# Kernel optimization log

Hardware: AMD Instinct MI355X
Metric: run time of the kernel (lower is better)

The kernel has to match this reference:

```python
import jax, jax.numpy as jnp
import numpy as np

N_EMBD = 1024
N_HEAD = 16


def setup_inputs() -> dict:
    key = jax.random.key(0)
    k1, k2, k3 = jax.random.split(key, 3)
    x = jax.random.normal(k1, (4, 2048, N_EMBD), dtype=jnp.float32)
    w_attn = jax.random.normal(k2, (N_EMBD, 3 * N_EMBD), dtype=jnp.float32) * (N_EMBD ** -0.5)
    w_proj = jax.random.normal(k3, (N_EMBD, N_EMBD), dtype=jnp.float32) * (N_EMBD ** -0.5)
    return {"x": x, "w_attn": w_attn, "w_proj": w_proj}


def reference(x, w_attn, w_proj):
    B, T, C = x.shape
    H = N_HEAD
    D = C // H  # head dim
    qkv = x @ w_attn  # [B,T,3C]
    q, k, v = jnp.split(qkv, 3, axis=-1)
    # [B,T,C] -> [B,H,T,D]
    q = q.reshape(B, T, H, D).transpose(0, 2, 1, 3)
    k = k.reshape(B, T, H, D).transpose(0, 2, 1, 3)
    v = v.reshape(B, T, H, D).transpose(0, 2, 1, 3)
    scale = 1.0 / jnp.sqrt(jnp.asarray(D, dtype=x.dtype))
    att = jnp.einsum('bhqd,bhkd->bhqk', q, k) * scale  # [B,H,T,T]
    causal = jnp.tril(jnp.ones((T, T), dtype=bool))
    att = jnp.where(causal, att, jnp.asarray(-jnp.inf, dtype=att.dtype))
    att = jax.nn.softmax(att, axis=-1)
    y = jnp.einsum('bhqk,bhkd->bhqd', att, v)  # [B,H,T,D]
    y = y.transpose(0, 2, 1, 3).reshape(B, T, C)
    return y @ w_proj
```

## Files before the change

### kernel.cpp

```cpp
#include <hip/hip_runtime.h>
#include <math.h>


typedef unsigned short ushort_t;
typedef __attribute__((ext_vector_type(8))) short bf16x8;
typedef __attribute__((ext_vector_type(4))) float f32x4;

#define MFMA16(a, b, c) __builtin_amdgcn_mfma_f32_16x16x32_bf16((a), (b), (c), 0, 0, 0)

#define CP_ASYNC16(lds, gp)                                                        \
    __builtin_amdgcn_global_load_lds(                                              \
        (const __attribute__((address_space(1))) void*)(gp),                       \
        (__attribute__((address_space(3))) void*)(lds), 16, 0, 0)

#define SCALE2 0.1803368801111204f

#define BAR() __builtin_amdgcn_s_barrier()
#define WAITBAR4()                                           \
    do {                                                     \
        asm volatile("s_waitcnt vmcnt(4)" ::: "memory");     \
        __builtin_amdgcn_s_barrier();                        \
    } while (0)
#define WAITBAR0()                                           \
    do {                                                     \
        asm volatile("s_waitcnt vmcnt(0)" ::: "memory");     \
        __builtin_amdgcn_s_barrier();                        \
    } while (0)

__device__ __forceinline__ ushort_t bf16r(float x) {
    unsigned int u = __float_as_uint(x);
    u += 0x7FFFu + ((u >> 16) & 1u);
    return (ushort_t)(u >> 16);
}

__device__ __forceinline__ unsigned cvt_pk_bf16(float lo, float hi) {
    unsigned r;
    asm("v_cvt_pk_bf16_f32 %0, %1, %2" : "=v"(r) : "v"(lo), "v"(hi));
    return r;
}
__device__ __forceinline__ void pl32_swap(unsigned& a, unsigned& c) {
    asm("v_permlane32_swap_b32 %0, %1" : "+v"(a), "+v"(c));
}
__device__ __forceinline__ void pl16_swap(unsigned& a, unsigned& c) {
    asm("v_permlane16_swap_b32 %0, %1" : "+v"(a), "+v"(c));
}


__global__ __launch_bounds__(256) void cast_f32_bf16(const float4* __restrict__ src,
                                                     ushort4* __restrict__ dst) {
    int i = blockIdx.x * 256 + threadIdx.x;
    float4 v = src[i];
    ushort4 o;
    o.x = bf16r(v.x); o.y = bf16r(v.y); o.z = bf16r(v.z); o.w = bf16r(v.w);
    dst[i] = o;
}

__global__ __launch_bounds__(256) void transpose_cast(const float* __restrict__ src,
                                                      ushort_t* __restrict__ dst,
                                                      int R, int Cc) {
    __shared__ float tile[32][33];
    const int tx = threadIdx.x, ty = threadIdx.y;
    const int c0 = blockIdx.x * 32, r0 = blockIdx.y * 32;
#pragma unroll
    for (int i = 0; i < 4; ++i)
        tile[ty + i * 8][tx] = src[(size_t)(r0 + ty + i * 8) * Cc + c0 + tx];
    __syncthreads();
#pragma unroll
    for (int i = 0; i < 4; ++i)
        dst[(size_t)(c0 + ty + i * 8) * R + r0 + tx] = bf16r(tile[tx][ty + i * 8]);
}

__global__ __launch_bounds__(512, 2)
void gemm256(const ushort_t* __restrict__ A, const ushort_t* __restrict__ Bt,
             int K, int mode,
             ushort_t* __restrict__ Qh, ushort_t* __restrict__ Kh,
             ushort_t* __restrict__ Vt, float* __restrict__ Cout, int nbx) {
    __shared__ __align__(16) ushort_t As[2][16384];
    __shared__ __align__(16) ushort_t Bs[2][16384];
    const int tid = threadIdx.x;
    const int l = tid & 63, w = tid >> 6;
    const int lm = l & 15, lq = l >> 4;
    const int wm = w >> 2, wn = w & 3;

    int bid = blockIdx.x;
    const int cpx = gridDim.x >> 3;
    bid = (bid & 7) * cpx + (bid >> 3);
    const int by = bid / nbx, bx = bid - by * nbx;
    const int row0 = by * 256, col0 = bx * 256;

    const int srow = tid >> 3, sslot = tid & 7;
    const int ssw = (sslot ^ (srow & 7)) * 8;
    const ushort_t* gA = A + (size_t)(row0 + srow) * K + ssw;
    const ushort_t* gB = Bt + (size_t)(col0 + srow) * K + ssw;

    auto stageA = [&](int dbuf, int hm, int T) {
        const ushort_t* s = gA + (size_t)(hm * 128) * K + T * 64;
        CP_ASYNC16(&As[dbuf][hm * 8192 + tid * 8], s);
        CP_ASYNC16(&As[dbuf][hm * 8192 + 4096 + tid * 8], s + (size_t)64 * K);
    };
    auto stageB = [&](int dbuf, int hm, int T) {
        const ushort_t* s = gB + (size_t)(hm * 128) * K + T * 64;
        CP_ASYNC16(&Bs[dbuf][hm * 8192 + tid * 8], s);
        CP_ASYNC16(&Bs[dbuf][hm * 8192 + 4096 + tid * 8], s + (size_t)64 * K);
    };

    const int arow0 = wm * 128 + lm;
    const int brow0 = wn * 64 + lm;
    const int lsw = lm & 7;

    f32x4 acc[8][4];
#pragma unroll
    for (int i = 0; i < 8; ++i)
#pragma unroll
        for (int j = 0; j < 4; ++j) acc[i][j] = (f32x4){0.f, 0.f, 0.f, 0.f};

    bf16x8 af[4][2];
    bf16x8 bq[2][2][2];

    auto ldA = [&](int d, int qm) {
#pragma unroll
        for (int mf = 0; mf < 4; ++mf) {
            const int r = arow0 + qm * 64 + mf * 16;
#pragma unroll
            for (int ks = 0; ks < 2; ++ks)
                af[mf][ks] =
                    *(const bf16x8*)(&As[d][r * 64 + (((ks << 2) | lq) ^ lsw) * 8]);
        }
    };
    auto ldB = [&](int d, int qn) {
#pragma unroll
        for (int nf = 0; nf < 2; ++nf) {
            const int r = brow0 + qn * 32 + nf * 16;
#pragma unroll
            for (int ks = 0; ks < 2; ++ks)
                bq[qn][nf][ks] =
                    *(const bf16x8*)(&Bs[d][r * 64 + (((ks << 2) | lq) ^ lsw) * 8]);
        }
    };
    auto mma = [&](int qm, int qn) {
        __builtin_amdgcn_s_setprio(1);
#pragma unroll
        for (int mf = 0; mf < 4; ++mf)
#pragma unroll
            for (int nf = 0; nf < 2; ++nf) {
                f32x4 c = acc[qm * 4 + mf][qn * 2 + nf];
                c = MFMA16(af[mf][0], bq[qn][nf][0], c);
                c = MFMA16(af[mf][1], bq[qn][nf][1], c);
                acc[qm * 4 + mf][qn * 2 + nf] = c;
            }
        __builtin_amdgcn_s_setprio(0);
    };

    stageA(0, 0, 0); stageA(0, 1, 0);
    stageB(0, 0, 0); stageB(0, 1, 0);
    stageB(1, 0, 1); stageB(1, 1, 1);

    const int ntiles = K >> 6;
    const int niter = ntiles >> 1;

    for (int it = 0; it < niter; ++it) {
        const int tE = 2 * it, tO = tE + 1;
        const bool s2 = (tE + 2) < ntiles;
        const bool s3 = (tE + 3) < ntiles;

        WAITBAR4();
        ldA(0, 0); ldB(0, 0);
        stageA(1, 0, tO);
        BAR();
        mma(0, 0);
        BAR();
        ldB(0, 1);
        stageA(1, 1, tO);
        BAR();
        mma(0, 1);
        BAR();
        ldA(0, 1);
        if (s2) stageB(0, 0, tE + 2);
        BAR();
        mma(1, 0);
        BAR();
        if (s2) stageB(0, 1, tE + 2);
        BAR();
        mma(1, 1);
        BAR();

        if (it + 1 < niter) { WAITBAR4(); } else { WAITBAR0(); }
        ldA(1, 0); ldB(1, 0);
        if (s2) stageA(0, 0, tE + 2);
        BAR();
        mma(0, 0);
        BAR();
        ldB(1, 1);
        if (s2) stageA(0, 1, tE + 2);
        BAR();
        mma(0, 1);
        BAR();
        ldA(1, 1);
        if (s3) stageB(1, 0, tE + 3);
        BAR();
        mma(1, 0);
        BAR();
        if (s3) stageB(1, 1, tE + 3);
        BAR();
        mma(1, 1);
        BAR();
    }

    if (mode == 1) {
#pragma unroll
        for (int im = 0; im < 8; ++im)
#pragma unroll
            for (int in = 0; in < 4; ++in)
#pragma unroll
                for (int reg = 0; reg < 4; ++reg) {
                    const int rr = row0 + wm * 128 + im * 16 + lq * 4 + reg;
                    const int cc = col0 + wn * 64 + in * 16 + lm;
                    Cout[(size_t)rr * 1024 + cc] = acc[im][in][reg];
                }
    } else {
#pragma unroll
        for (int im = 0; im < 8; ++im) {
#pragma unroll
            for (int in = 0; in < 4; ++in) {
#pragma unroll
                for (int reg = 0; reg < 4; ++reg) {
                    const int rr = row0 + wm * 128 + im * 16 + lq * 4 + reg;
                    const int cc = col0 + wn * 64 + in * 16 + lm;
                    const float v = acc[im][in][reg];
                    const int b = rr >> 11, t = rr & 2047;
                    if (cc < 1024) {
                        const int h = cc >> 6, d = cc & 63;
                        Qh[((size_t)(b * 16 + h) * 2048 + t) * 64 + d] =
                            bf16r(v * SCALE2);
                    } else if (cc < 2048) {
                        const int c2 = cc - 1024, h = c2 >> 6, d = c2 & 63;
                        Kh[((size_t)(b * 16 + h) * 2048 + t) * 64 + d] = bf16r(v);
                    } else {
                        const int c2 = cc - 2048, h = c2 >> 6, d = c2 & 63;
                        Vt[((size_t)(b * 16 + h) * 64 + d) * 2048 + t] = bf16r(v);
                    }
                }
            }
        }
    }
}

__global__ __launch_bounds__(256, 4)
void attn_mfma(const ushort_t* __restrict__ Qh, const ushort_t* __restrict__ Kh,
               const ushort_t* __restrict__ Vt, ushort_t* __restrict__ Y) {
    __shared__ ushort_t Ks[2][4096];
    __shared__ ushort_t Vs[2][4096];
    const int tid = threadIdx.x, l = tid & 63, w = tid >> 6;
    const int lm = l & 15, lq = l >> 4;
    const int bh = blockIdx.x;
    const int pr = blockIdx.y;
    const int qbA = pr, qbB = 31 - pr;
    const int b = bh >> 4, h = bh & 15;
    const f32x4 zero4 = {0.f, 0.f, 0.f, 0.f};
    const short oneb = (short)0x3F80;
    const bf16x8 onesf = {oneb, oneb, oneb, oneb, oneb, oneb, oneb, oneb};
    const int lqs8 = (lq ^ ((lm >> 1) & 3)) * 8;

    bf16x8 qf[2][2];
    {
        const ushort_t* qA = Qh + ((size_t)bh * 2048 + qbA * 64 + w * 16 + lm) * 64 + lq * 8;
        const ushort_t* qB = Qh + ((size_t)bh * 2048 + qbB * 64 + w * 16 + lm) * 64 + lq * 8;
        qf[0][0] = *(const bf16x8*)(qA);
        qf[0][1] = *(const bf16x8*)(qA + 32);
        qf[1][0] = *(const bf16x8*)(qB);
        qf[1][1] = *(const bf16x8*)(qB + 32);
    }

    f32x4 O[2][4], Ol[2];
#pragma unroll
    for (int q = 0; q < 2; ++q) {
        Ol[q] = zero4;
#pragma unroll
        for (int i = 0; i < 4; ++i) O[q][i] = zero4;
    }

    const int srow = tid >> 2, slot = tid & 3;
    const int srcoff = ((slot ^ ((srow >> 1) & 3)) * 8);
    const ushort_t* gKr = Kh + ((size_t)bh * 2048 + srow) * 64 + srcoff;
    const ushort_t* gVr = Vt + ((size_t)bh * 64 + srow) * 2048 + srcoff;

    auto prefetch = [&](int jbn, int dbuf) {
        const ushort_t* gk = gKr + (size_t)jbn * 4096;
        const ushort_t* gv = gVr + jbn * 64;
        CP_ASYNC16(&Ks[dbuf][tid * 8], gk);
        CP_ASYNC16(&Ks[dbuf][2048 + tid * 8], gk + 32);
        CP_ASYNC16(&Vs[dbuf][tid * 8], gv);
        CP_ASYNC16(&Vs[dbuf][2048 + tid * 8], gv + 32);
    };

    auto process = [&](const bf16x8 (&kf)[4][2], const ushort_t* Vb,
                       const bf16x8 (&qfr)[2], f32x4 (&Or)[4], f32x4& Olr,
                       bool diag) {
        f32x4 st[4];
        __builtin_amdgcn_s_setprio(1);
#pragma unroll
        for (int n = 0; n < 4; ++n) {
            f32x4 s_acc = zero4;
            s_acc = MFMA16(kf[n][0], qfr[0], s_acc);
            s_acc = MFMA16(kf[n][1], qfr[1], s_acc);
            st[n] = s_acc;
        }
        __builtin_amdgcn_s_setprio(0);

        float p[4][4];
#pragma unroll
        for (int n = 0; n < 4; ++n)
#pragma unroll
            for (int reg = 0; reg < 4; ++reg)
                p[n][reg] = __builtin_amdgcn_exp2f(st[n][reg]);
        if (diag) {
            const int qloc = w * 16 + lm;
#pragma unroll
            for (int n = 0; n < 4; ++n)
#pragma unroll
                for (int reg = 0; reg < 4; ++reg)
                    if (n * 16 + lq * 4 + reg > qloc) p[n][reg] = 0.f;
        }

        unsigned cpk[4][2];
#pragma unroll
        for (int n = 0; n < 4; ++n) {
            cpk[n][0] = cvt_pk_bf16(p[n][0], p[n][1]);
            cpk[n][1] = cvt_pk_bf16(p[n][2], p[n][3]);
        }

        union U8 { unsigned u[4]; bf16x8 v; };
        bf16x8 pf0, pf1;
        {
            unsigned z00 = cpk[0][0], z10 = cpk[1][0];
            unsigned z01 = cpk[0][1], z11 = cpk[1][1];
            pl32_swap(z00, z10); pl16_swap(z00, z10);
            pl32_swap(z01, z11); pl16_swap(z01, z11);
            U8 t0; t0.u[0] = z00; t0.u[1] = z01; t0.u[2] = z10; t0.u[3] = z11;
            pf0 = t0.v;
            unsigned y00 = cpk[2][0], y10 = cpk[3][0];
            unsigned y01 = cpk[2][1], y11 = cpk[3][1];
            pl32_swap(y00, y10); pl16_swap(y00, y10);
            pl32_swap(y01, y11); pl16_swap(y01, y11);
            U8 t1; t1.u[0] = y00; t1.u[1] = y01; t1.u[2] = y10; t1.u[3] = y11;
            pf1 = t1.v;
        }

        __builtin_amdgcn_s_setprio(1);
#pragma unroll
        for (int dn = 0; dn < 4; ++dn) {
            const bf16x8 vf0 = *(const bf16x8*)(Vb + (dn * 16 + lm) * 32 + lqs8);
            const bf16x8 vf1 = *(const bf16x8*)(Vb + 2048 + (dn * 16 + lm) * 32 + lqs8);
            Or[dn] = MFMA16(pf0, vf0, Or[dn]);
            Or[dn] = MFMA16(pf1, vf1, Or[dn]);
        }
        Olr = MFMA16(pf0, onesf, Olr);
        Olr = MFMA16(pf1, onesf, Olr);
        __builtin_amdgcn_s_setprio(0);
    };

    prefetch(0, 0);
    for (int jb = 0; jb <= qbB; ++jb) {
        const int buf = jb & 1;
        __syncthreads();
        if (jb < qbB) prefetch(jb + 1, buf ^ 1);

        const ushort_t* Kb = Ks[buf];
        const ushort_t* Vb = Vs[buf];
        bf16x8 kf[4][2];
#pragma unroll
        for (int n = 0; n < 4; ++n) {
            kf[n][0] = *(const bf16x8*)(Kb + (n * 16 + lm) * 32 + lqs8);
            kf[n][1] = *(const bf16x8*)(Kb + 2048 + (n * 16 + lm) * 32 + lqs8);
        }

        process(kf, Vb, qf[1], O[1], Ol[1], jb == qbB);
        if (jb <= qbA)
            process(kf, Vb, qf[0], O[0], Ol[0], jb == qbA);
    }

#pragma unroll
    for (int qs = 0; qs < 2; ++qs) {
        const int tq = (qs ? qbB : qbA) * 64;
#pragma unroll
        for (int reg = 0; reg < 4; ++reg) {
            const float inv = 1.f / Ol[qs][reg];
            const size_t row = (size_t)b * 2048 + tq + w * 16 + lq * 4 + reg;
#pragma unroll
            for (int dn = 0; dn < 4; ++dn)
                Y[row * 1024 + h * 64 + dn * 16 + lm] = bf16r(O[qs][dn][reg] * inv);
        }
    }
}


extern "C" void kernel_launch(void* const* d_in, const int* in_sizes, int n_in,
                              void* d_out, int out_size, void* d_ws, size_t ws_size,
                              hipStream_t stream) {
    const float* x      = (const float*)d_in[0];
    const float* w_attn = (const float*)d_in[1];
    const float* w_proj = (const float*)d_in[2];
    float* out = (float*)d_out;

    char* ws = (char*)d_ws;
    ushort_t* xb   = (ushort_t*)(ws);
    ushort_t* watT = (ushort_t*)(ws + 16777216);
    ushort_t* wpjT = (ushort_t*)(ws + 23068672);
    ushort_t* Qh   = (ushort_t*)(ws + 25165824);
    ushort_t* Kh   = (ushort_t*)(ws + 41943040);
    ushort_t* Vt   = (ushort_t*)(ws + 58720256);
    ushort_t* Y    = (ushort_t*)(ws + 75497472);

    hipLaunchKernelGGL(cast_f32_bf16, dim3(8192), dim3(256), 0, stream,
                       (const float4*)x, (ushort4*)xb);
    hipLaunchKernelGGL(transpose_cast, dim3(96, 32), dim3(32, 8), 0, stream,
                       w_attn, watT, 1024, 3072);
    hipLaunchKernelGGL(transpose_cast, dim3(32, 32), dim3(32, 8), 0, stream,
                       w_proj, wpjT, 1024, 1024);

    hipLaunchKernelGGL(gemm256, dim3(384), dim3(512), 0, stream,
                       xb, watT, 1024, 0, Qh, Kh, Vt, (float*)nullptr, 12);

    hipLaunchKernelGGL(attn_mfma, dim3(64, 16), dim3(256), 0, stream,
                       Qh, Kh, Vt, Y);

    hipLaunchKernelGGL(gemm256, dim3(128), dim3(512), 0, stream,
                       Y, wpjT, 1024, 1, (ushort_t*)nullptr, (ushort_t*)nullptr,
                       (ushort_t*)nullptr, out, 4);
}
```

Baseline: 263.3 us.

## Shrink GEMM tile to 256x128 with eight-phase pipeline to fill more CUs

Halves the GEMM block tile width from 256 to 128 columns, doubling the number of blocks for both the QKV and output projections, and restructures the wave layout and per-iteration phases (fewer barriers per K-tile). The aim is to occupy more compute units, especially for the output projection which previously launched only 128 blocks. It trades away some operand reuse per block and increases total global traffic for the A operand.

```diff
diff --git a/kernel.cpp b/kernel.cpp
--- a/kernel.cpp
+++ b/kernel.cpp
@@ -16,9 +16,9 @@
 #define SCALE2 0.1803368801111204f
 
 #define BAR() __builtin_amdgcn_s_barrier()
-#define WAITBAR4()                                           \
+#define WAITBAR2()                                           \
     do {                                                     \
-        asm volatile("s_waitcnt vmcnt(4)" ::: "memory");     \
+        asm volatile("s_waitcnt vmcnt(2)" ::: "memory");     \
         __builtin_amdgcn_s_barrier();                        \
     } while (0)
 #define WAITBAR0()                                           \
@@ -71,22 +71,22 @@
 }
 
 __global__ __launch_bounds__(512, 2)
-void gemm256(const ushort_t* __restrict__ A, const ushort_t* __restrict__ Bt,
-             int K, int mode,
-             ushort_t* __restrict__ Qh, ushort_t* __restrict__ Kh,
-             ushort_t* __restrict__ Vt, float* __restrict__ Cout, int nbx) {
+void gemm_8ph(const ushort_t* __restrict__ A, const ushort_t* __restrict__ Bt,
+              int K, int mode,
+              ushort_t* __restrict__ Qh, ushort_t* __restrict__ Kh,
+              ushort_t* __restrict__ Vt, float* __restrict__ Cout, int nbx) {
     __shared__ __align__(16) ushort_t As[2][16384];
-    __shared__ __align__(16) ushort_t Bs[2][16384];
+    __shared__ __align__(16) ushort_t Bs[2][8192];
     const int tid = threadIdx.x;
     const int l = tid & 63, w = tid >> 6;
     const int lm = l & 15, lq = l >> 4;
-    const int wm = w >> 2, wn = w & 3;
+    const int wm = w >> 1, wn = w & 1;
 
     int bid = blockIdx.x;
     const int cpx = gridDim.x >> 3;
     bid = (bid & 7) * cpx + (bid >> 3);
     const int by = bid / nbx, bx = bid - by * nbx;
-    const int row0 = by * 256, col0 = bx * 256;
+    const int row0 = by * 256, col0 = bx * 128;
 
     const int srow = tid >> 3, sslot = tid & 7;
     const int ssw = (sslot ^ (srow & 7)) * 8;
@@ -98,62 +98,66 @@
         CP_ASYNC16(&As[dbuf][hm * 8192 + tid * 8], s);
         CP_ASYNC16(&As[dbuf][hm * 8192 + 4096 + tid * 8], s + (size_t)64 * K);
     };
-    auto stageB = [&](int dbuf, int hm, int T) {
-        const ushort_t* s = gB + (size_t)(hm * 128) * K + T * 64;
-        CP_ASYNC16(&Bs[dbuf][hm * 8192 + tid * 8], s);
-        CP_ASYNC16(&Bs[dbuf][hm * 8192 + 4096 + tid * 8], s + (size_t)64 * K);
-    };
-
-    const int arow0 = wm * 128 + lm;
+    auto stageB = [&](int dbuf, int T) {
+        const ushort_t* s = gB + T * 64;
+        CP_ASYNC16(&Bs[dbuf][tid * 8], s);
+        CP_ASYNC16(&Bs[dbuf][4096 + tid * 8], s + (size_t)64 * K);
+    };
+
+    const int arow0 = wm * 64 + lm;
     const int brow0 = wn * 64 + lm;
     const int lsw = lm & 7;
 
-    f32x4 acc[8][4];
-#pragma unroll
-    for (int i = 0; i < 8; ++i)
+    f32x4 acc[4][4];
+#pragma unroll
+    for (int i = 0; i < 4; ++i)
 #pragma unroll
         for (int j = 0; j < 4; ++j) acc[i][j] = (f32x4){0.f, 0.f, 0.f, 0.f};
 
-    bf16x8 af[4][2];
+    bf16x8 af[2][2];
     bf16x8 bq[2][2][2];
 
     auto ldA = [&](int d, int qm) {
 #pragma unroll
-        for (int mf = 0; mf < 4; ++mf) {
-            const int r = arow0 + qm * 64 + mf * 16;
+        for (int mf = 0; mf < 2; ++mf) {
+            const int r = arow0 + qm * 32 + mf * 16;
 #pragma unroll
             for (int ks = 0; ks < 2; ++ks)
                 af[mf][ks] =
                     *(const bf16x8*)(&As[d][r * 64 + (((ks << 2) | lq) ^ lsw) * 8]);
         }
     };
-    auto ldB = [&](int d, int qn) {
-#pragma unroll
-        for (int nf = 0; nf < 2; ++nf) {
-            const int r = brow0 + qn * 32 + nf * 16;
-#pragma unroll
-            for (int ks = 0; ks < 2; ++ks)
-                bq[qn][nf][ks] =
-                    *(const bf16x8*)(&Bs[d][r * 64 + (((ks << 2) | lq) ^ lsw) * 8]);
-        }
-    };
-    auto mma = [&](int qm, int qn) {
+    auto ldB = [&](int d) {
+#pragma unroll
+        for (int qn = 0; qn < 2; ++qn)
+#pragma unroll
+            for (int nf = 0; nf < 2; ++nf) {
+                const int r = brow0 + qn * 32 + nf * 16;
+#pragma unroll
+                for (int ks = 0; ks < 2; ++ks)
+                    bq[qn][nf][ks] =
+                        *(const bf16x8*)(&Bs[d][r * 64 + (((ks << 2) | lq) ^ lsw) * 8]);
+            }
+    };
+    auto mma = [&](int qm) {
         __builtin_amdgcn_s_setprio(1);
 #pragma unroll
-        for (int mf = 0; mf < 4; ++mf)
-#pragma unroll
-            for (int nf = 0; nf < 2; ++nf) {
-                f32x4 c = acc[qm * 4 + mf][qn * 2 + nf];
-                c = MFMA16(af[mf][0], bq[qn][nf][0], c);
-                c = MFMA16(af[mf][1], bq[qn][nf][1], c);
-                acc[qm * 4 + mf][qn * 2 + nf] = c;
-            }
+        for (int mf = 0; mf < 2; ++mf)
+#pragma unroll
+            for (int qn = 0; qn < 2; ++qn)
+#pragma unroll
+                for (int nf = 0; nf < 2; ++nf) {
+                    f32x4 c = acc[qm * 2 + mf][qn * 2 + nf];
+                    c = MFMA16(af[mf][0], bq[qn][nf][0], c);
+                    c = MFMA16(af[mf][1], bq[qn][nf][1], c);
+                    acc[qm * 2 + mf][qn * 2 + nf] = c;
+                }
         __builtin_amdgcn_s_setprio(0);
     };
 
     stageA(0, 0, 0); stageA(0, 1, 0);
-    stageB(0, 0, 0); stageB(0, 1, 0);
-    stageB(1, 0, 1); stageB(1, 1, 1);
+    stageB(0, 0);
+    stageB(1, 1);
 
     const int ntiles = K >> 6;
     const int niter = ntiles >> 1;
@@ -163,70 +167,54 @@
         const bool s2 = (tE + 2) < ntiles;
         const bool s3 = (tE + 3) < ntiles;
 
-        WAITBAR4();
-        ldA(0, 0); ldB(0, 0);
+        WAITBAR2();
+        ldA(0, 0); ldB(0);
         stageA(1, 0, tO);
         BAR();
-        mma(0, 0);
-        BAR();
-        ldB(0, 1);
+        mma(0);
+        BAR();
+        ldA(0, 1);
         stageA(1, 1, tO);
-        BAR();
-        mma(0, 1);
-        BAR();
-        ldA(0, 1);
-        if (s2) stageB(0, 0, tE + 2);
-        BAR();
-        mma(1, 0);
-        BAR();
-        if (s2) stageB(0, 1, tE + 2);
-        BAR();
-        mma(1, 1);
-        BAR();
-
-        if (it + 1 < niter) { WAITBAR4(); } else { WAITBAR0(); }
-        ldA(1, 0); ldB(1, 0);
+        if (s2) stageB(0, tE + 2);
+        BAR();
+        mma(1);
+        BAR();
+
+        if (it + 1 < niter) { WAITBAR2(); } else { WAITBAR0(); }
+        ldA(1, 0); ldB(1);
         if (s2) stageA(0, 0, tE + 2);
         BAR();
-        mma(0, 0);
-        BAR();
-        ldB(1, 1);
+        mma(0);
+        BAR();
+        ldA(1, 1);
         if (s2) stageA(0, 1, tE + 2);
-        BAR();
-        mma(0, 1);
-        BAR();
-        ldA(1, 1);
-        if (s3) stageB(1, 0, tE + 3);
-        BAR();
-        mma(1, 0);
-        BAR();
-        if (s3) stageB(1, 1, tE + 3);
-        BAR();
-        mma(1, 1);
+        if (s3) stageB(1, tE + 3);
+        BAR();
+        mma(1);
         BAR();
     }
 
     if (mode == 1) {
 #pragma unroll
-        for (int im = 0; im < 8; ++im)
-#pragma unroll
-            for (int in = 0; in < 4; ++in)
+        for (int im = 0; im < 4; ++im)
+#pragma unroll
+            for (int jn = 0; jn < 4; ++jn)
 #pragma unroll
                 for (int reg = 0; reg < 4; ++reg) {
-                    const int rr = row0 + wm * 128 + im * 16 + lq * 4 + reg;
-                    const int cc = col0 + wn * 64 + in * 16 + lm;
-                    Cout[(size_t)rr * 1024 + cc] = acc[im][in][reg];
+                    const int rr = row0 + wm * 64 + im * 16 + lq * 4 + reg;
+                    const int cc = col0 + wn * 64 + jn * 16 + lm;
+                    Cout[(size_t)rr * 1024 + cc] = acc[im][jn][reg];
                 }
     } else {
 #pragma unroll
-        for (int im = 0; im < 8; ++im) {
-#pragma unroll
-            for (int in = 0; in < 4; ++in) {
+        for (int im = 0; im < 4; ++im) {
+#pragma unroll
+            for (int jn = 0; jn < 4; ++jn) {
 #pragma unroll
                 for (int reg = 0; reg < 4; ++reg) {
-                    const int rr = row0 + wm * 128 + im * 16 + lq * 4 + reg;
-                    const int cc = col0 + wn * 64 + in * 16 + lm;
-                    const float v = acc[im][in][reg];
+                    const int rr = row0 + wm * 64 + im * 16 + lq * 4 + reg;
+                    const int cc = col0 + wn * 64 + jn * 16 + lm;
+                    const float v = acc[im][jn][reg];
                     const int b = rr >> 11, t = rr & 2047;
                     if (cc < 1024) {
                         const int h = cc >> 6, d = cc & 63;
@@ -418,13 +406,13 @@
     hipLaunchKernelGGL(transpose_cast, dim3(32, 32), dim3(32, 8), 0, stream,
                        w_proj, wpjT, 1024, 1024);
 
-    hipLaunchKernelGGL(gemm256, dim3(384), dim3(512), 0, stream,
-                       xb, watT, 1024, 0, Qh, Kh, Vt, (float*)nullptr, 12);
+    hipLaunchKernelGGL(gemm_8ph, dim3(768), dim3(512), 0, stream,
+                       xb, watT, 1024, 0, Qh, Kh, Vt, (float*)nullptr, 24);
 
     hipLaunchKernelGGL(attn_mfma, dim3(64, 16), dim3(256), 0, stream,
                        Qh, Kh, Vt, Y);
 
-    hipLaunchKernelGGL(gemm256, dim3(128), dim3(512), 0, stream,
+    hipLaunchKernelGGL(gemm_8ph, dim3(256), dim3(512), 0, stream,
                        Y, wpjT, 1024, 1, (ushort_t*)nullptr, (ushort_t*)nullptr,
-                       (ushort_t*)nullptr, out, 4);
-}
+                       (ushort_t*)nullptr, out, 8);
+}
```

Measured after the change: 246.8 us. 6.3% less time.
